# Performance work log

Measured on AMD Instinct MI355X. Metric: run time of the kernel, lower is better.

Reference implementation:

```python
import jax, jax.numpy as jnp
import numpy as np

# Sizes: N nodes, E directed edges, C input channels, H hidden channels.
N = 50000
E = 800000
C = 64
H = 64
EPS = 1e-5


def _bn(h, gamma, beta):
    # LazyBatchNorm: per-channel normalization over all rows (batch stats).
    m = h.mean(axis=0)
    v = ((h - m) ** 2).mean(axis=0)
    return (h - m) * jax.lax.rsqrt(v + EPS) * gamma + beta


def setup_inputs() -> dict:
    key = jax.random.key(0)
    ks = jax.random.split(key, 8)

    def glorot(k, shape):
        return jax.random.normal(k, shape, dtype=jnp.float32) / jnp.sqrt(jnp.float32(shape[0]))

    x = jax.random.normal(ks[0], (N, C), dtype=jnp.float32)
    edge_index = jax.random.randint(ks[1], (2, E), 0, N)
    return {
        "x": x,
        "edge_index": edge_index,
        "W_unite": glorot(ks[2], (2 * C, H)),
        "b_unite": jnp.zeros((H,), jnp.float32),
        "g1": jnp.ones((H,), jnp.float32),
        "be1": jnp.zeros((H,), jnp.float32),
        "W_gconv": glorot(ks[3], (2 * H, H)),
        "b_gconv": jnp.zeros((H,), jnp.float32),
        "g2": jnp.ones((H,), jnp.float32),
        "be2": jnp.zeros((H,), jnp.float32),
        "W_transfer": glorot(ks[4], (2 * H, H)),
        "b_transfer": jnp.zeros((H,), jnp.float32),
        "W_lin": glorot(ks[5], (H, H)),
        "b_lin": jnp.zeros((H,), jnp.float32),
        "g3": jnp.ones((H,), jnp.float32),
        "be3": jnp.zeros((H,), jnp.float32),
    }


def reference(x, edge_index, W_unite, b_unite, g1, be1, W_gconv, b_gconv, g2, be2,
              W_transfer, b_transfer, W_lin, b_lin, g3, be3):
    n = x.shape[0]
    src_e = edge_index[0]
    dst_e = edge_index[1]
    # linmaps1: ptensors0 -> ptensors1 with singleton reference domains (identity on data).
    # unite1: each node's domain becomes {node} U N(node). Row layout: first n rows
    # are self rows (atom i in domain i), then E rows (atom src in domain dst).
    self_idx = jnp.arange(n)
    rows_src = jnp.concatenate([self_idx, src_e])   # atom index per row
    rows_dom = jnp.concatenate([self_idx, dst_e])   # domain owner per row

    # --- unite1 (2 linmaps: gather + broadcast-of-domain-sum), then linear + BN + relu
    f = x[rows_src]                                           # [R, C] gather
    dsum = jax.ops.segment_sum(f, rows_dom, num_segments=n)   # [N, C]
    h = jnp.concatenate([f, dsum[rows_dom]], axis=-1) @ W_unite + b_unite  # [R, H]
    h = jax.nn.relu(_bn(h, g1, be1))
    # dropout1: identity in eval mode

    # --- higher graph conv: reduce each domain to order-0, aggregate over edges,
    # broadcast back and combine with local rows (2 maps), linear + BN + relu
    s = jax.ops.segment_sum(h, rows_dom, num_segments=n)          # [N, H] per-domain reduce
    msg = jax.ops.segment_sum(s[src_e], dst_e, num_segments=n)    # [N, H] neighborhood sum
    h2 = jnp.concatenate([h, msg[rows_dom]], axis=-1) @ W_gconv + b_gconv  # [R, H]
    h2 = jax.nn.relu(_bn(h2, g2, be2))
    # dropout2: identity

    # --- transfer back to ptensors0 (singleton domains): per-atom reduce over all rows
    # referencing that atom + the atom's own self row (2 maps), linear + BN + relu.
    # NOTE: the source reuses batchnorm2 here (it is assigned twice in __init__).
    agg = jax.ops.segment_sum(h2, rows_src, num_segments=n)       # [N, H]
    t = jnp.concatenate([h2[:n], agg], axis=-1) @ W_transfer + b_transfer  # [N, H]
    t = jax.nn.relu(_bn(t, g2, be2))
    # dropout3: identity

    # --- final linear + relu, BN + relu
    out = jax.nn.relu(t @ W_lin + b_lin)
    out = jax.nn.relu(_bn(out, g3, be3))
    # dropout4: identity
    return out
```

## Files before the change

kernel.cpp:

```cpp
#include <hip/hip_runtime.h>
#include <cstdint>
#include <math.h>

#define NN 50000
#define EE 800000
#define RR 850000
#define NT_N 3125
#define NT_R 53125
#define NBLK_H2 2048
#define NBLK_MM 512
#define CHUNK 512
#define NCH 98

typedef short  bf16x8 __attribute__((ext_vector_type(8)));
typedef float  f32x4  __attribute__((ext_vector_type(4)));

__device__ __forceinline__ float bf2f(unsigned short b) {
    unsigned int u = ((unsigned int)b) << 16;
    return __builtin_bit_cast(float, u);
}
__device__ __forceinline__ unsigned short f2bf(float f) {
    unsigned int u = __builtin_bit_cast(unsigned int, f);
    u = u + 0x7fffu + ((u >> 16) & 1u);
    return (unsigned short)(u >> 16);
}
__device__ __forceinline__ void atomAddD(double* p, double v) { unsafeAtomicAdd(p, v); }
__device__ __forceinline__ int atomAddI(int* p, int v) { return atomicAdd(p, v); }

__device__ __forceinline__ void split8(const float* p, bf16x8& hi, bf16x8& lo) {
    f32x4 v0 = *reinterpret_cast<const f32x4*>(p);
    f32x4 v1 = *reinterpret_cast<const f32x4*>(p + 4);
#pragma unroll
    for (int j = 0; j < 4; j++) {
        unsigned short h0 = f2bf(v0[j]);
        hi[j] = (short)h0; lo[j] = (short)f2bf(v0[j] - bf2f(h0));
        unsigned short h1 = f2bf(v1[j]);
        hi[4 + j] = (short)h1; lo[4 + j] = (short)f2bf(v1[j] - bf2f(h1));
    }
}
__device__ __forceinline__ void split8r(const float* v, bf16x8& hi, bf16x8& lo) {
#pragma unroll
    for (int j = 0; j < 8; j++) {
        unsigned short h = f2bf(v[j]);
        hi[j] = (short)h; lo[j] = (short)f2bf(v[j] - bf2f(h));
    }
}

template <bool RELU, bool STATS>
__device__ __forceinline__ void epi_tile(float* wl, int lane, const f32x4* acc,
                                         const float* bv, float* __restrict__ gout,
                                         int tile, double* ssum, double* ssq) {
    const int m = lane & 15, quad = lane >> 4;
#pragma unroll
    for (int ct = 0; ct < 4; ct++)
#pragma unroll
        for (int i = 0; i < 4; i++) {
            float val = acc[ct][i] + bv[ct];
            if (RELU) val = fmaxf(val, 0.f);
            wl[(quad * 4 + i) * 68 + ct * 16 + m] = val;
            if (STATS) { ssum[ct] += (double)val; ssq[ct] += (double)val * (double)val; }
        }
    asm volatile("s_waitcnt lgkmcnt(0)" ::: "memory");
#pragma unroll
    for (int j = 0; j < 4; j++) {
        int row = j * 4 + quad;
        f32x4 vv = *reinterpret_cast<const f32x4*>(wl + row * 68 + m * 4);
        *reinterpret_cast<f32x4*>(gout + ((size_t)(tile << 4) + row) * 64 + m * 4) = vv;
    }
}

__device__ __forceinline__ void epi_tile_b16(float* wl, int lane, const f32x4* acc,
                                             unsigned short* __restrict__ gout, int tile) {
    const int m = lane & 15, quad = lane >> 4;
#pragma unroll
    for (int ct = 0; ct < 4; ct++)
#pragma unroll
        for (int i = 0; i < 4; i++)
            wl[(quad * 4 + i) * 68 + ct * 16 + m] = acc[ct][i];
    asm volatile("s_waitcnt lgkmcnt(0)" ::: "memory");
#pragma unroll
    for (int j = 0; j < 4; j++) {
        int row = j * 4 + quad;
        f32x4 vv = *reinterpret_cast<const f32x4*>(wl + row * 68 + m * 4);
        unsigned int p0 = (unsigned int)f2bf(vv[0]) | ((unsigned int)f2bf(vv[1]) << 16);
        unsigned int p1 = (unsigned int)f2bf(vv[2]) | ((unsigned int)f2bf(vv[3]) << 16);
        uint2 pk; pk.x = p0; pk.y = p1;
        *reinterpret_cast<uint2*>(gout + ((size_t)(tile << 4) + row) * 64 + m * 4) = pk;
    }
}

__device__ __forceinline__ void stats_block_out(float* ldsbase, int lane, int wid,
                                                const double* ssum, const double* ssq,
                                                double* __restrict__ part) {
    const int m = lane & 15, quad = lane >> 4;
    double* dl = (double*)ldsbase;
    __syncthreads();
#pragma unroll
    for (int ct = 0; ct < 4; ct++) {
        double sv = ssum[ct], qv = ssq[ct];
        sv += __shfl_xor(sv, 16, 64); sv += __shfl_xor(sv, 32, 64);
        qv += __shfl_xor(qv, 16, 64); qv += __shfl_xor(qv, 32, 64);
        if (quad == 0) {
            dl[wid * 128 + ct * 16 + m]      = sv;
            dl[wid * 128 + 64 + ct * 16 + m] = qv;
        }
    }
    __syncthreads();
    int tid = wid * 64 + lane;
    if (tid < 128) {
        double tot = dl[tid] + dl[128 + tid] + dl[256 + tid] + dl[384 + tid];
        part[(size_t)blockIdx.x * 128 + tid] = tot;
    }
}

__global__ void k_red(const double* __restrict__ p, int nblk, double* __restrict__ raw) {
    int t = threadIdx.x;
    double acc = 0.0;
    for (int b = blockIdx.x; b < nblk; b += gridDim.x)
        acc += p[(size_t)b * 128 + t];
    atomAddD(&raw[t], acc);
}

__global__ void k_deg(const int* __restrict__ ei, int* __restrict__ od, int* __restrict__ id) {
    int e = blockIdx.x * 256 + threadIdx.x;
    atomAddI(&od[ei[e]], 1);
    atomAddI(&id[ei[EE + e]], 1);
}

__global__ void k_xc(const float* __restrict__ x, unsigned short* __restrict__ xb) {
    int i = blockIdx.x * 256 + threadIdx.x;
    xb[i] = f2bf(x[i]);
}

__global__ void k_scanA(const int* __restrict__ id, const int* __restrict__ od,
                        int* __restrict__ csum) {
    int arr = blockIdx.x / NCH;
    int ch  = blockIdx.x % NCH;
    const int* cnt = arr ? od : id;
    int t = threadIdx.x;
    int i0 = ch * CHUNK + t;
    int s = 0;
    if (i0 < NN) s += cnt[i0];
    if (i0 + 256 < NN && (t + 256) < CHUNK) s += cnt[i0 + 256];
#pragma unroll
    for (int d = 1; d < 64; d <<= 1) s += __shfl_xor(s, d, 64);
    __shared__ int ws[4];
    if ((t & 63) == 0) ws[t >> 6] = s;
    __syncthreads();
    if (t == 0) csum[arr * NCH + ch] = ws[0] + ws[1] + ws[2] + ws[3];
}

__global__ void k_scanB(int* __restrict__ csum) {
    __shared__ int part[256];
    int t = threadIdx.x;
    int arr = t >> 7, slot = t & 127;
    int v = (slot < NCH) ? csum[arr * NCH + slot] : 0;
    part[t] = v;
    __syncthreads();
#pragma unroll
    for (int d = 1; d < 128; d <<= 1) {
        int val = (slot >= d) ? part[t - d] : 0;
        __syncthreads();
        part[t] += val;
        __syncthreads();
    }
    if (slot < NCH)
        csum[arr * NCH + slot] = (slot == 0) ? 0 : part[t - 1];
}

__global__ void k_scanC(const int* __restrict__ id, const int* __restrict__ od,
                        const int* __restrict__ csum,
                        int* __restrict__ off, int* __restrict__ cursor,
                        int* __restrict__ off_s, int* __restrict__ cursor_s) {
    int arr = blockIdx.x / NCH;
    int ch  = blockIdx.x % NCH;
    const int* cnt = arr ? od : id;
    int* o  = arr ? off_s : off;
    int* cu = arr ? cursor_s : cursor;
    int t = threadIdx.x;
    int idx = ch * CHUNK + 2 * t;
    int e0 = 0, e1 = 0;
    if (idx < NN)     e0 = cnt[idx];
    if (idx + 1 < NN) e1 = cnt[idx + 1];
    int p = e0 + e1;
    int lane = t & 63;
    int incl = p;
#pragma unroll
    for (int d = 1; d < 64; d <<= 1) {
        int v = __shfl_up(incl, d, 64);
        if (lane >= d) incl += v;
    }
    __shared__ int wsum[4];
    if (lane == 63) wsum[t >> 6] = incl;
    __syncthreads();
    int w = t >> 6;
    int wbase = 0;
#pragma unroll
    for (int i = 0; i < 4; i++) if (i < w) wbase += wsum[i];
    int base = csum[arr * NCH + ch] + wbase + (incl - p);
    if (idx < NN)     { o[idx]     = base;      cu[idx]     = base; }
    if (idx + 1 < NN) { o[idx + 1] = base + e0; cu[idx + 1] = base + e0; }
    if (blockIdx.x == 0 && t == 0) { off[NN] = EE; off_s[NN] = EE; }
}

__global__ void k_fill(const int* __restrict__ ei, int* __restrict__ cursor,
                       unsigned int* __restrict__ sd_s) {
    int e = blockIdx.x * 256 + threadIdx.x;
    int s = ei[e], d = ei[EE + e];
    int p = atomAddI(&cursor[d], 1);
    sd_s[p] = (unsigned int)s | ((unsigned int)d << 16);
}

__global__ void k_fill2(const unsigned int* __restrict__ sd_s, int* __restrict__ cursor_s,
                        int* __restrict__ perm_s) {
    int p = blockIdx.x * 256 + threadIdx.x;
    int s = (int)(sd_s[p] & 0xFFFFu);
    int q = atomAddI(&cursor_s[s], 1);
    perm_s[q] = p;
}

__global__ void k_dsum_csr(const float* __restrict__ x, const unsigned short* __restrict__ xb,
                           const int* __restrict__ off,
                           const unsigned int* __restrict__ sd_s, float* __restrict__ dsum) {
    int team = (blockIdx.x * 256 + threadIdx.x) >> 6;
    int c = threadIdx.x & 63;
    float a[16];
#pragma unroll
    for (int j = 0; j < 16; j++) a[j] = 0.f;
    a[0] = x[(size_t)team * 64 + c];
    int e = off[team], e1 = off[team + 1];
    for (; e + 15 < e1; e += 16)
#pragma unroll
        for (int j = 0; j < 16; j++) a[j] += bf2f(xb[(size_t)(sd_s[e + j] & 0xFFFFu) * 64 + c]);
    for (; e + 3 < e1; e += 4)
#pragma unroll
        for (int j = 0; j < 4; j++) a[j] += bf2f(xb[(size_t)(sd_s[e + j] & 0xFFFFu) * 64 + c]);
    for (; e < e1; e++) a[0] += bf2f(xb[(size_t)(sd_s[e] & 0xFFFFu) * 64 + c]);
#pragma unroll
    for (int j = 0; j < 8; j++) a[j] += a[j + 8];
#pragma unroll
    for (int j = 0; j < 4; j++) a[j] += a[j + 4];
    dsum[(size_t)team * 64 + c] = (a[0] + a[1]) + (a[2] + a[3]);
}

__global__ void k_uv3(const float* __restrict__ x, const float* __restrict__ dsum,
                      const float* __restrict__ W, unsigned short* __restrict__ ub,
                      float* __restrict__ v, float* __restrict__ u2) {
    __shared__ float lds[4][16 * 68];
    const int lane = threadIdx.x & 63;
    const int wid = threadIdx.x >> 6;
    const int m = lane & 15, quad = lane >> 4;
    const int gwave = (blockIdx.x * blockDim.x + threadIdx.x) >> 6;
    const int nwaves = (gridDim.x * blockDim.x) >> 6;
    float* wl = lds[wid];

    bf16x8 wfh[4][4], wfl[4][4];
#pragma unroll
    for (int kk = 0; kk < 4; kk++)
#pragma unroll
        for (int ct = 0; ct < 4; ct++) {
            float wv[8];
#pragma unroll
            for (int j = 0; j < 8; j++)
                wv[j] = W[(kk * 32 + quad * 8 + j) * 64 + ct * 16 + m];
            split8r(wv, wfh[kk][ct], wfl[kk][ct]);
        }
    float zb[4] = {0.f, 0.f, 0.f, 0.f};

    for (int tile = gwave; tile < NT_N; tile += nwaves) {
        const int r = (tile << 4) + m;
        bf16x8 ah[4], al[4];
        split8(x    + (size_t)r * 64 + quad * 8,      ah[0], al[0]);
        split8(x    + (size_t)r * 64 + 32 + quad * 8, ah[1], al[1]);
        split8(dsum + (size_t)r * 64 + quad * 8,      ah[2], al[2]);
        split8(dsum + (size_t)r * 64 + 32 + quad * 8, ah[3], al[3]);

        f32x4 zero = {0.f, 0.f, 0.f, 0.f};
        f32x4 aU[4], aV[4], aU2[4];
#pragma unroll
        for (int ct = 0; ct < 4; ct++) {
            aU[ct] = zero; aV[ct] = zero; aU2[ct] = zero;
#pragma unroll
            for (int kk = 0; kk < 2; kk++) {
                aU[ct]  = __builtin_amdgcn_mfma_f32_16x16x32_bf16(al[kk],   wfh[kk][ct],   aU[ct],  0, 0, 0);
                aU[ct]  = __builtin_amdgcn_mfma_f32_16x16x32_bf16(ah[kk],   wfl[kk][ct],   aU[ct],  0, 0, 0);
                aU[ct]  = __builtin_amdgcn_mfma_f32_16x16x32_bf16(ah[kk],   wfh[kk][ct],   aU[ct],  0, 0, 0);
                aV[ct]  = __builtin_amdgcn_mfma_f32_16x16x32_bf16(al[kk+2], wfh[kk+2][ct], aV[ct],  0, 0, 0);
                aV[ct]  = __builtin_amdgcn_mfma_f32_16x16x32_bf16(ah[kk+2], wfl[kk+2][ct], aV[ct],  0, 0, 0);
                aV[ct]  = __builtin_amdgcn_mfma_f32_16x16x32_bf16(ah[kk+2], wfh[kk+2][ct], aV[ct],  0, 0, 0);
                aU2[ct] = __builtin_amdgcn_mfma_f32_16x16x32_bf16(al[kk+2], wfh[kk][ct],   aU2[ct], 0, 0, 0);
                aU2[ct] = __builtin_amdgcn_mfma_f32_16x16x32_bf16(ah[kk+2], wfl[kk][ct],   aU2[ct], 0, 0, 0);
                aU2[ct] = __builtin_amdgcn_mfma_f32_16x16x32_bf16(ah[kk+2], wfh[kk][ct],   aU2[ct], 0, 0, 0);
            }
        }
        epi_tile_b16(wl, lane, aU, ub, tile);
        epi_tile<false, false>(wl, lane, aV,  zb, v,  tile, nullptr, nullptr);
        epi_tile<false, false>(wl, lane, aU2, zb, u2, tile, nullptr, nullptr);
    }
}

__global__ void k_stats1a(const unsigned short* __restrict__ ub, const float* __restrict__ v,
                          const float* __restrict__ u2, const int* __restrict__ od,
                          const int* __restrict__ id, double* __restrict__ stats_raw) {
    __shared__ double lsum[4][64], lsq[4][64];
    int tid = threadIdx.x, c = tid & 63, w = tid >> 6;
    double a1 = 0.0, a2 = 0.0;
    for (int n = blockIdx.x * 4 + w; n < NN; n += gridDim.x * 4) {
        double uu = (double)bf2f(ub[(size_t)n * 64 + c]);
        double vv = v[(size_t)n * 64 + c];
        double uu2 = u2[(size_t)n * 64 + c];
        double wod = 1.0 + od[n], wid = 1.0 + id[n];
        a1 += wod * uu + wid * vv;
        a2 += wod * uu * uu + wid * vv * vv + 2.0 * vv * uu2;
    }
    lsum[w][c] = a1; lsq[w][c] = a2;
    __syncthreads();
    if (w == 0) {
        a1 = lsum[0][c] + lsum[1][c] + lsum[2][c] + lsum[3][c];
        a2 = lsq[0][c] + lsq[1][c] + lsq[2][c] + lsq[3][c];
        atomAddD(&stats_raw[c], a1);
        atomAddD(&stats_raw[64 + c], a2);
    }
}

__global__ void k_fin1(const double* __restrict__ raw, const float* __restrict__ b,
                       float* __restrict__ fin, double inv_cnt) {
    int c = threadIdx.x;
    double m1 = raw[c] * inv_cnt;
    double var = raw[64 + c] * inv_cnt - m1 * m1;
    if (var < 0.0) var = 0.0;
    fin[c] = (float)(m1 + (double)b[c]);
    fin[64 + c] = (float)(1.0 / sqrt(var + 1e-5));
}

__global__ void k_fin(const double* __restrict__ raw, float* __restrict__ fin, double inv_cnt) {
    int c = threadIdx.x;
    double mean = raw[c] * inv_cnt;
    double var = raw[64 + c] * inv_cnt - mean * mean;
    if (var < 0.0) var = 0.0;
    fin[c] = (float)mean;
    fin[64 + c] = (float)(1.0 / sqrt(var + 1e-5));
}

__global__ void k_s1h(const unsigned short* __restrict__ ub, const float* __restrict__ v,
                      const int* __restrict__ off, const unsigned int* __restrict__ sd_s,
                      const float* __restrict__ b_un, const float* __restrict__ fin,
                      const float* __restrict__ g1, const float* __restrict__ be1,
                      unsigned short* __restrict__ stb, unsigned short* __restrict__ hb) {
    int team = (blockIdx.x * 256 + threadIdx.x) >> 6;
    int c = threadIdx.x & 63;
    float sc = fin[64 + c] * g1[c];
    float tsh = (b_un[c] - fin[c]) * sc + be1[c];
    float vn = v[(size_t)team * 64 + c];
    float a[16];
#pragma unroll
    for (int j = 0; j < 16; j++) a[j] = 0.f;
    float hs = fmaxf((bf2f(ub[(size_t)team * 64 + c]) + vn) * sc + tsh, 0.f);
    a[0] = hs;
    hb[(size_t)team * 64 + c] = f2bf(hs);
    int e = off[team], e1 = off[team + 1];
    for (; e + 15 < e1; e += 16)
#pragma unroll
        for (int j = 0; j < 16; j++) {
            float h = fmaxf((bf2f(ub[(size_t)(sd_s[e + j] & 0xFFFFu) * 64 + c]) + vn) * sc + tsh, 0.f);
            a[j] += h;
            hb[(size_t)(NN + e + j) * 64 + c] = f2bf(h);
        }
    for (; e + 3 < e1; e += 4)
#pragma unroll
        for (int j = 0; j < 4; j++) {
            float h = fmaxf((bf2f(ub[(size_t)(sd_s[e + j] & 0xFFFFu) * 64 + c]) + vn) * sc + tsh, 0.f);
            a[j] += h;
            hb[(size_t)(NN + e + j) * 64 + c] = f2bf(h);
        }
    for (; e < e1; e++) {
        float h = fmaxf((bf2f(ub[(size_t)(sd_s[e] & 0xFFFFu) * 64 + c]) + vn) * sc + tsh, 0.f);
        a[0] += h;
        hb[(size_t)(NN + e) * 64 + c] = f2bf(h);
    }
#pragma unroll
    for (int j = 0; j < 8; j++) a[j] += a[j + 8];
#pragma unroll
    for (int j = 0; j < 4; j++) a[j] += a[j + 4];
    stb[(size_t)team * 64 + c] = f2bf((a[0] + a[1]) + (a[2] + a[3]));
}

__global__ void k_msg_csr(const int* __restrict__ off, const unsigned int* __restrict__ sd_s,
                          const unsigned short* __restrict__ stb, float* __restrict__ msg) {
    int team = (blockIdx.x * 256 + threadIdx.x) >> 6;
    int c = threadIdx.x & 63;
    float a[16];
#pragma unroll
    for (int j = 0; j < 16; j++) a[j] = 0.f;
    int e = off[team], e1 = off[team + 1];
    for (; e + 15 < e1; e += 16)
#pragma unroll
        for (int j = 0; j < 16; j++) a[j] += bf2f(stb[(size_t)(sd_s[e + j] & 0xFFFFu) * 64 + c]);
    for (; e + 3 < e1; e += 4)
#pragma unroll
        for (int j = 0; j < 4; j++) a[j] += bf2f(stb[(size_t)(sd_s[e + j] & 0xFFFFu) * 64 + c]);
    for (; e < e1; e++) a[0] += bf2f(stb[(size_t)(sd_s[e] & 0xFFFFu) * 64 + c]);
#pragma unroll
    for (int j = 0; j < 8; j++) a[j] += a[j + 8];
#pragma unroll
    for (int j = 0; j < 4; j++) a[j] += a[j + 4];
    msg[(size_t)team * 64 + c] = (a[0] + a[1]) + (a[2] + a[3]);
}

__global__ void k_mb(const float* __restrict__ in, float* __restrict__ outp,
                     const float* __restrict__ W) {
    __shared__ float lds[4][16 * 68];
    const int lane = threadIdx.x & 63;
    const int wid = threadIdx.x >> 6;
    const int m = lane & 15, quad = lane >> 4;
    const int gwave = (blockIdx.x * blockDim.x + threadIdx.x) >> 6;
    const int nwaves = (gridDim.x * blockDim.x) >> 6;
    float* wl = lds[wid];

    bf16x8 wfh[2][4], wfl[2][4];
#pragma unroll
    for (int kk = 0; kk < 2; kk++)
#pragma unroll
        for (int ct = 0; ct < 4; ct++) {
            float wv[8];
#pragma unroll
            for (int j = 0; j < 8; j++)
                wv[j] = W[(kk * 32 + quad * 8 + j) * 64 + ct * 16 + m];
            split8r(wv, wfh[kk][ct], wfl[kk][ct]);
        }
    float zb[4] = {0.f, 0.f, 0.f, 0.f};

    for (int tile = gwave; tile < NT_N; tile += nwaves) {
        const int r = (tile << 4) + m;
        bf16x8 ah[2], al[2];
        split8(in + (size_t)r * 64 + quad * 8,      ah[0], al[0]);
        split8(in + (size_t)r * 64 + 32 + quad * 8, ah[1], al[1]);

        f32x4 zero = {0.f, 0.f, 0.f, 0.f};
        f32x4 acc[4];
#pragma unroll
        for (int ct = 0; ct < 4; ct++) {
            acc[ct] = zero;
#pragma unroll
            for (int kk = 0; kk < 2; kk++) {
                acc[ct] = __builtin_amdgcn_mfma_f32_16x16x32_bf16(al[kk], wfh[kk][ct], acc[ct], 0, 0, 0);
                acc[ct] = __builtin_amdgcn_mfma_f32_16x16x32_bf16(ah[kk], wfl[kk][ct], acc[ct], 0, 0, 0);
                acc[ct] = __builtin_amdgcn_mfma_f32_16x16x32_bf16(ah[kk], wfh[kk][ct], acc[ct], 0, 0, 0);
            }
        }
        epi_tile<false, false>(wl, lane, acc, zb, outp, tile, nullptr, nullptr);
    }
}

__global__ void k_h2(const unsigned short* __restrict__ hb, unsigned short* __restrict__ h2b,
                     const float* __restrict__ mb, const unsigned int* __restrict__ sd_s,
                     const float* __restrict__ W, const float* __restrict__ b_gc,
                     double* __restrict__ part) {
    __shared__ float lds[4][16 * 68];
    const int lane = threadIdx.x & 63;
    const int wid = threadIdx.x >> 6;
    const int m = lane & 15, quad = lane >> 4;
    const int gwave = (blockIdx.x * blockDim.x + threadIdx.x) >> 6;
    const int nwaves = (gridDim.x * blockDim.x) >> 6;
    float* wl = lds[wid];

    bf16x8 wfh[2][4], wfl[2][4];
#pragma unroll
    for (int kk = 0; kk < 2; kk++)
#pragma unroll
        for (int ct = 0; ct < 4; ct++) {
            float wv[8];
#pragma unroll
            for (int j = 0; j < 8; j++)
                wv[j] = W[(kk * 32 + quad * 8 + j) * 64 + ct * 16 + m];
            split8r(wv, wfh[kk][ct], wfl[kk][ct]);
        }

    float bv[4];
#pragma unroll
    for (int ct = 0; ct < 4; ct++) bv[ct] = b_gc[ct * 16 + m];

    double ssum[4] = {0,0,0,0}, ssq[4] = {0,0,0,0};

    for (int tile = gwave; tile < NT_R; tile += nwaves) {
        const int r = (tile << 4) + m;
        int dm = (tile < NT_N) ? r : (int)(sd_s[r - NN] >> 16);

        bf16x8 ah[2];
        ah[0] = *reinterpret_cast<const bf16x8*>(hb + (size_t)r * 64 + quad * 8);
        ah[1] = *reinterpret_cast<const bf16x8*>(hb + (size_t)r * 64 + 32 + quad * 8);

        f32x4 zero = {0.f, 0.f, 0.f, 0.f};
        f32x4 acc[4];
#pragma unroll
        for (int ct = 0; ct < 4; ct++) {
            acc[ct] = zero;
#pragma unroll
            for (int kk = 0; kk < 2; kk++) {
                acc[ct] = __builtin_amdgcn_mfma_f32_16x16x32_bf16(ah[kk], wfl[kk][ct], acc[ct], 0, 0, 0);
                acc[ct] = __builtin_amdgcn_mfma_f32_16x16x32_bf16(ah[kk], wfh[kk][ct], acc[ct], 0, 0, 0);
            }
        }

#pragma unroll
        for (int i = 0; i < 4; i++) {
            int dmv = __shfl(dm, (lane & 48) + quad * 4 + i, 64);
#pragma unroll
            for (int ct = 0; ct < 4; ct++) {
                float val = acc[ct][i] + bv[ct] + mb[(size_t)dmv * 64 + ct * 16 + m];
                wl[(quad * 4 + i) * 68 + ct * 16 + m] = val;
                ssum[ct] += (double)val;
                ssq[ct]  += (double)val * (double)val;
            }
        }
        asm volatile("s_waitcnt lgkmcnt(0)" ::: "memory");
#pragma unroll
        for (int j = 0; j < 4; j++) {
            int row = j * 4 + quad;
            f32x4 vv = *reinterpret_cast<const f32x4*>(wl + row * 68 + m * 4);
            unsigned int p0 = (unsigned int)f2bf(vv[0]) | ((unsigned int)f2bf(vv[1]) << 16);
            unsigned int p1 = (unsigned int)f2bf(vv[2]) | ((unsigned int)f2bf(vv[3]) << 16);
            uint2 pk; pk.x = p0; pk.y = p1;
            *reinterpret_cast<uint2*>(h2b + ((size_t)(tile << 4) + row) * 64 + m * 4) = pk;
        }
    }

    stats_block_out(&lds[0][0], lane, wid, ssum, ssq, part);
}

__global__ void k_agg_csr(const unsigned short* __restrict__ h2b, const int* __restrict__ off_s,
                          const int* __restrict__ perm_s, const float* __restrict__ fin2,
                          const float* __restrict__ g2, const float* __restrict__ be2,
                          float* __restrict__ agg) {
    int n = (blockIdx.x * 256 + threadIdx.x) >> 6;
    int c = threadIdx.x & 63;
    float sc = fin2[64 + c] * g2[c];
    float sh = be2[c] - fin2[c] * sc;
    float a[16];
#pragma unroll
    for (int j = 0; j < 16; j++) a[j] = 0.f;
    a[0] = fmaxf(bf2f(h2b[(size_t)n * 64 + c]) * sc + sh, 0.f);
    int q = off_s[n], q1 = off_s[n + 1];
    for (; q + 15 < q1; q += 16)
#pragma unroll
        for (int j = 0; j < 16; j++) {
            float hv = bf2f(h2b[(size_t)(NN + perm_s[q + j]) * 64 + c]);
            a[j] += fmaxf(hv * sc + sh, 0.f);
        }
    for (; q + 3 < q1; q += 4)
#pragma unroll
        for (int j = 0; j < 4; j++) {
            float hv = bf2f(h2b[(size_t)(NN + perm_s[q + j]) * 64 + c]);
            a[j] += fmaxf(hv * sc + sh, 0.f);
        }
    for (; q < q1; q++) {
        float hv = bf2f(h2b[(size_t)(NN + perm_s[q]) * 64 + c]);
        a[0] += fmaxf(hv * sc + sh, 0.f);
    }
#pragma unroll
    for (int j = 0; j < 8; j++) a[j] += a[j + 8];
#pragma unroll
    for (int j = 0; j < 4; j++) a[j] += a[j + 4];
    agg[(size_t)n * 64 + c] = (a[0] + a[1]) + (a[2] + a[3]);
}

__global__ void k_mm3(const unsigned short* __restrict__ h2b, const float* __restrict__ agg,
                      const float* __restrict__ W, const float* __restrict__ bias,
                      const float* __restrict__ fin2, const float* __restrict__ g2,
                      const float* __restrict__ be2,
                      float* __restrict__ outp, double* __restrict__ part) {
    __shared__ float lds[4][16 * 68];
    const int lane = threadIdx.x & 63;
    const int wid = threadIdx.x >> 6;
    const int m = lane & 15, quad = lane >> 4;
    const int gwave = (blockIdx.x * blockDim.x + threadIdx.x) >> 6;
    const int nwaves = (gridDim.x * blockDim.x) >> 6;
    float* wl = lds[wid];

    bf16x8 wfh[4][4], wfl[4][4];
#pragma unroll
    for (int kk = 0; kk < 4; kk++)
#pragma unroll
        for (int ct = 0; ct < 4; ct++) {
            float wv[8];
#pragma unroll
            for (int j = 0; j < 8; j++)
                wv[j] = W[(kk * 32 + quad * 8 + j) * 64 + ct * 16 + m];
            split8r(wv, wfh[kk][ct], wfl[kk][ct]);
        }

    float bv[4];
#pragma unroll
    for (int ct = 0; ct < 4; ct++) bv[ct] = bias[ct * 16 + m];

    float s2f[2][8], t2f[2][8];
#pragma unroll
    for (int kk = 0; kk < 2; kk++)
#pragma unroll
        for (int j = 0; j < 8; j++) {
            int c = kk * 32 + quad * 8 + j;
            float sc = fin2[64 + c] * g2[c];
            s2f[kk][j] = sc;
            t2f[kk][j] = be2[c] - fin2[c] * sc;
        }

    double ssum[4] = {0,0,0,0}, ssq[4] = {0,0,0,0};

    for (int tile = gwave; tile < NT_N; tile += nwaves) {
        const int r = (tile << 4) + m;
        bf16x8 ah[4], al[4];
#pragma unroll
        for (int kk = 0; kk < 2; kk++) {
            bf16x8 hv = *reinterpret_cast<const bf16x8*>(h2b + (size_t)r * 64 + kk * 32 + quad * 8);
            float tv[8];
#pragma unroll
            for (int j = 0; j < 8; j++) {
                float f = bf2f((unsigned short)hv[j]);
                tv[j] = fmaxf(f * s2f[kk][j] + t2f[kk][j], 0.f);
            }
            split8r(tv, ah[kk], al[kk]);
        }
        split8(agg + (size_t)r * 64 + quad * 8,      ah[2], al[2]);
        split8(agg + (size_t)r * 64 + 32 + quad * 8, ah[3], al[3]);

        f32x4 zero = {0.f, 0.f, 0.f, 0.f};
        f32x4 acc[4];
#pragma unroll
        for (int ct = 0; ct < 4; ct++) {
            acc[ct] = zero;
#pragma unroll
            for (int kk = 0; kk < 4; kk++)
                acc[ct] = __builtin_amdgcn_mfma_f32_16x16x32_bf16(al[kk], wfh[kk][ct], acc[ct], 0, 0, 0);
#pragma unroll
            for (int kk = 0; kk < 4; kk++)
                acc[ct] = __builtin_amdgcn_mfma_f32_16x16x32_bf16(ah[kk], wfl[kk][ct], acc[ct], 0, 0, 0);
#pragma unroll
            for (int kk = 0; kk < 4; kk++)
                acc[ct] = __builtin_amdgcn_mfma_f32_16x16x32_bf16(ah[kk], wfh[kk][ct], acc[ct], 0, 0, 0);
        }

        epi_tile<false, true>(wl, lane, acc, bv, outp, tile, ssum, ssq);
    }

    stats_block_out(&lds[0][0], lane, wid, ssum, ssq, part);
}

__global__ void k_mm4(const float* __restrict__ tpre, const float* __restrict__ W,
                      const float* __restrict__ bias, const float* __restrict__ fin3,
                      const float* __restrict__ g2, const float* __restrict__ be2,
                      float* __restrict__ outp, double* __restrict__ part) {
    __shared__ float lds[4][16 * 68];
    const int lane = threadIdx.x & 63;
    const int wid = threadIdx.x >> 6;
    const int m = lane & 15, quad = lane >> 4;
    const int gwave = (blockIdx.x * blockDim.x + threadIdx.x) >> 6;
    const int nwaves = (gridDim.x * blockDim.x) >> 6;
    float* wl = lds[wid];

    bf16x8 wfh[2][4], wfl[2][4];
#pragma unroll
    for (int kk = 0; kk < 2; kk++)
#pragma unroll
        for (int ct = 0; ct < 4; ct++) {
            float wv[8];
#pragma unroll
            for (int j = 0; j < 8; j++)
                wv[j] = W[(kk * 32 + quad * 8 + j) * 64 + ct * 16 + m];
            split8r(wv, wfh[kk][ct], wfl[kk][ct]);
        }

    float bv[4];
#pragma unroll
    for (int ct = 0; ct < 4; ct++) bv[ct] = bias[ct * 16 + m];

    float sc[2][8], sh[2][8];
#pragma unroll
    for (int kk = 0; kk < 2; kk++)
#pragma unroll
        for (int j = 0; j < 8; j++) {
            int c = kk * 32 + quad * 8 + j;
            float s = fin3[64 + c] * g2[c];
            sc[kk][j] = s;
            sh[kk][j] = be2[c] - fin3[c] * s;
        }

    double ssum[4] = {0,0,0,0}, ssq[4] = {0,0,0,0};

    for (int tile = gwave; tile < NT_N; tile += nwaves) {
        const int r = (tile << 4) + m;
        bf16x8 ah[2], al[2];
#pragma unroll
        for (int kk = 0; kk < 2; kk++) {
            f32x4 v0 = *reinterpret_cast<const f32x4*>(tpre + (size_t)r * 64 + kk * 32 + quad * 8);
            f32x4 v1 = *reinterpret_cast<const f32x4*>(tpre + (size_t)r * 64 + kk * 32 + quad * 8 + 4);
            float tv[8];
#pragma unroll
            for (int j = 0; j < 4; j++) {
                tv[j]     = fmaxf(v0[j] * sc[kk][j]     + sh[kk][j],     0.f);
                tv[4 + j] = fmaxf(v1[j] * sc[kk][4 + j] + sh[kk][4 + j], 0.f);
            }
            split8r(tv, ah[kk], al[kk]);
        }

        f32x4 zero = {0.f, 0.f, 0.f, 0.f};
        f32x4 acc[4];
#pragma unroll
        for (int ct = 0; ct < 4; ct++) {
            acc[ct] = zero;
#pragma unroll
            for (int kk = 0; kk < 2; kk++) {
                acc[ct] = __builtin_amdgcn_mfma_f32_16x16x32_bf16(al[kk], wfh[kk][ct], acc[ct], 0, 0, 0);
                acc[ct] = __builtin_amdgcn_mfma_f32_16x16x32_bf16(ah[kk], wfl[kk][ct], acc[ct], 0, 0, 0);
                acc[ct] = __builtin_amdgcn_mfma_f32_16x16x32_bf16(ah[kk], wfh[kk][ct], acc[ct], 0, 0, 0);
            }
        }

        epi_tile<true, true>(wl, lane, acc, bv, outp, tile, ssum, ssq);
    }

    stats_block_out(&lds[0][0], lane, wid, ssum, ssq, part);
}

__global__ void k_out(const float* __restrict__ op, const float* __restrict__ fin,
                      const float* __restrict__ g, const float* __restrict__ be,
                      float* __restrict__ out) {
    int i = blockIdx.x * 256 + threadIdx.x;
    int c = i & 63;
    out[i] = fmaxf((op[i] - fin[c]) * fin[64 + c] * g[c] + be[c], 0.f);
}

extern "C" void kernel_launch(void* const* d_in, const int* in_sizes, int n_in,
                              void* d_out, int out_size, void* d_ws, size_t ws_size,
                              hipStream_t stream) {
    const float* x    = (const float*)d_in[0];
    const int*   ei   = (const int*)d_in[1];
    const float* W_un = (const float*)d_in[2];
    const float* b_un = (const float*)d_in[3];
    const float* g1   = (const float*)d_in[4];
    const float* be1  = (const float*)d_in[5];
    const float* W_gc = (const float*)d_in[6];
    const float* b_gc = (const float*)d_in[7];
    const float* g2   = (const float*)d_in[8];
    const float* be2  = (const float*)d_in[9];
    const float* W_tr = (const float*)d_in[10];
    const float* b_tr = (const float*)d_in[11];
    const float* W_li = (const float*)d_in[12];
    const float* b_li = (const float*)d_in[13];
    const float* g3   = (const float*)d_in[14];
    const float* be3  = (const float*)d_in[15];

    float* ws = (float*)d_ws;
    const size_t FN = (size_t)NN * 64;
    const size_t FR = (size_t)RR * 64;
    float* P0 = ws;
    float* P1 = ws + FN;
    float* P2 = ws + 2 * FN;
    float* H  = ws + 3 * FN;
    unsigned short* ub   = (unsigned short*)P0;
    float* v      = P1;
    unsigned short* stb  = (unsigned short*)P2;
    int*   csum   = (int*)P2;
    float* dsum   = H;
    float* u2     = H + FN;
    unsigned short* xb16 = (unsigned short*)(H + 2 * FN);
    unsigned short* hb  = (unsigned short*)H;
    unsigned short* h2b = (unsigned short*)H + FR;
    float* msg    = P0;
    float* agg    = P1;
    float* tpre   = P2;
    float* outpre = P0;
    double* part_h2 = (double*)P2;
    double* part_m3 = (double*)P0;
    double* part_m4 = (double*)P1;
    double*       stats_raw = (double*)(H + FR);
    int*          od        = (int*)(stats_raw + 512);
    int*          id        = od + NN;
    int*          off       = id + NN;
    int*          cursor    = off + NN + 1;
    int*          off_s     = cursor + NN;
    int*          cursor_s  = off_s + NN + 1;
    unsigned int* sd_s      = (unsigned int*)(cursor_s + NN);
    int*          perm_s    = (int*)(sd_s + EE);
    float*        stats_fin = (float*)(perm_s + EE);

    hipMemsetAsync(stats_raw, 0, 512 * sizeof(double) + 2 * NN * sizeof(int), stream);

    k_deg  <<<3125, 256, 0, stream>>>(ei, od, id);
    k_xc   <<<12500, 256, 0, stream>>>(x, xb16);
    k_scanA<<<2 * NCH, 256, 0, stream>>>(id, od, csum);
    k_scanB<<<1, 256, 0, stream>>>(csum);
    k_scanC<<<2 * NCH, 256, 0, stream>>>(id, od, csum, off, cursor, off_s, cursor_s);
    k_fill <<<3125, 256, 0, stream>>>(ei, cursor, sd_s);
    k_fill2<<<3125, 256, 0, stream>>>(sd_s, cursor_s, perm_s);

    k_dsum_csr<<<12500, 256, 0, stream>>>(x, xb16, off, sd_s, dsum);
    k_uv3<<<512, 256, 0, stream>>>(x, dsum, W_un, ub, v, u2);

    k_stats1a<<<256, 256, 0, stream>>>(ub, v, u2, od, id, stats_raw + 0);
    k_fin1<<<1, 64, 0, stream>>>(stats_raw + 0, b_un, stats_fin + 0, 1.0 / (double)RR);
    k_s1h<<<12500, 256, 0, stream>>>(ub, v, off, sd_s, b_un, stats_fin + 0, g1, be1,
                                     stb, hb);
    k_msg_csr<<<12500, 256, 0, stream>>>(off, sd_s, stb, msg);
    k_mb<<<512, 256, 0, stream>>>(msg, msg, W_gc + 64 * 64);

    k_h2<<<NBLK_H2, 256, 0, stream>>>(hb, h2b, msg, sd_s, W_gc, b_gc, part_h2);
    k_red<<<32, 128, 0, stream>>>(part_h2, NBLK_H2, stats_raw + 128);
    k_fin<<<1, 64, 0, stream>>>(stats_raw + 128, stats_fin + 128, 1.0 / (double)RR);
    k_agg_csr<<<12500, 256, 0, stream>>>(h2b, off_s, perm_s, stats_fin + 128, g2, be2, agg);

    k_mm3<<<NBLK_MM, 256, 0, stream>>>(h2b, agg, W_tr, b_tr, stats_fin + 128, g2, be2,
                                       tpre, part_m3);
    k_red<<<16, 128, 0, stream>>>(part_m3, NBLK_MM, stats_raw + 256);
    k_fin<<<1, 64, 0, stream>>>(stats_raw + 256, stats_fin + 256, 1.0 / (double)NN);

    k_mm4<<<NBLK_MM, 256, 0, stream>>>(tpre, W_li, b_li, stats_fin + 256, g2, be2,
                                       outpre, part_m4);
    k_red<<<16, 128, 0, stream>>>(part_m4, NBLK_MM, stats_raw + 384);
    k_fin<<<1, 64, 0, stream>>>(stats_raw + 384, stats_fin + 384, 1.0 / (double)NN);

    k_out<<<12500, 256, 0, stream>>>(outpre, stats_fin + 384, g3, be3, (float*)d_out);
}
```

Before: 716.7 us.

## Fuse degree count with bf16 convert, fold BN1 stats into uv3, store agg as bf16

```diff
diff --git a/kernel.cpp b/kernel.cpp
--- a/kernel.cpp
+++ b/kernel.cpp
@@ -121,15 +121,14 @@
     atomAddD(&raw[t], acc);
 }
 
-__global__ void k_deg(const int* __restrict__ ei, int* __restrict__ od, int* __restrict__ id) {
-    int e = blockIdx.x * 256 + threadIdx.x;
-    atomAddI(&od[ei[e]], 1);
-    atomAddI(&id[ei[EE + e]], 1);
-}
-
-__global__ void k_xc(const float* __restrict__ x, unsigned short* __restrict__ xb) {
+__global__ void k_degx(const int* __restrict__ ei, int* __restrict__ od, int* __restrict__ id,
+                       const float* __restrict__ x, unsigned short* __restrict__ xb) {
     int i = blockIdx.x * 256 + threadIdx.x;
     xb[i] = f2bf(x[i]);
+    if (i < EE) {
+        atomAddI(&od[ei[i]], 1);
+        atomAddI(&id[ei[EE + i]], 1);
+    }
 }
 
 __global__ void k_scanA(const int* __restrict__ id, const int* __restrict__ od,
@@ -244,15 +243,17 @@
 }
 
 __global__ void k_uv3(const float* __restrict__ x, const float* __restrict__ dsum,
-                      const float* __restrict__ W, unsigned short* __restrict__ ub,
-                      float* __restrict__ v, float* __restrict__ u2) {
+                      const float* __restrict__ W,
+                      const int* __restrict__ od, const int* __restrict__ id,
+                      unsigned short* __restrict__ ub, float* __restrict__ v,
+                      double* __restrict__ part) {
     __shared__ float lds[4][16 * 68];
     const int lane = threadIdx.x & 63;
-    const int wid = threadIdx.x >> 6;
+    const int wid_ = threadIdx.x >> 6;
     const int m = lane & 15, quad = lane >> 4;
     const int gwave = (blockIdx.x * blockDim.x + threadIdx.x) >> 6;
     const int nwaves = (gridDim.x * blockDim.x) >> 6;
-    float* wl = lds[wid];
+    float* wl = lds[wid_];
 
     bf16x8 wfh[4][4], wfl[4][4];
 #pragma unroll
@@ -266,6 +267,7 @@
             split8r(wv, wfh[kk][ct], wfl[kk][ct]);
         }
     float zb[4] = {0.f, 0.f, 0.f, 0.f};
+    double ssum[4] = {0,0,0,0}, ssq[4] = {0,0,0,0};
 
     for (int tile = gwave; tile < NT_N; tile += nwaves) {
         const int r = (tile << 4) + m;
@@ -293,34 +295,24 @@
                 aU2[ct] = __builtin_amdgcn_mfma_f32_16x16x32_bf16(ah[kk+2], wfh[kk][ct],   aU2[ct], 0, 0, 0);
             }
         }
+
+#pragma unroll
+        for (int i = 0; i < 4; i++) {
+            int r2 = (tile << 4) + quad * 4 + i;
+            double wod = 1.0 + od[r2], wgt = 1.0 + id[r2];
+#pragma unroll
+            for (int ct = 0; ct < 4; ct++) {
+                double uu = aU[ct][i], vv = aV[ct][i], u2v = aU2[ct][i];
+                ssum[ct] += wod * uu + wgt * vv;
+                ssq[ct]  += wod * uu * uu + wgt * vv * vv + 2.0 * vv * u2v;
+            }
+        }
+
         epi_tile_b16(wl, lane, aU, ub, tile);
-        epi_tile<false, false>(wl, lane, aV,  zb, v,  tile, nullptr, nullptr);
-        epi_tile<false, false>(wl, lane, aU2, zb, u2, tile, nullptr, nullptr);
-    }
-}
-
-__global__ void k_stats1a(const unsigned short* __restrict__ ub, const float* __restrict__ v,
-                          const float* __restrict__ u2, const int* __restrict__ od,
-                          const int* __restrict__ id, double* __restrict__ stats_raw) {
-    __shared__ double lsum[4][64], lsq[4][64];
-    int tid = threadIdx.x, c = tid & 63, w = tid >> 6;
-    double a1 = 0.0, a2 = 0.0;
-    for (int n = blockIdx.x * 4 + w; n < NN; n += gridDim.x * 4) {
-        double uu = (double)bf2f(ub[(size_t)n * 64 + c]);
-        double vv = v[(size_t)n * 64 + c];
-        double uu2 = u2[(size_t)n * 64 + c];
-        double wod = 1.0 + od[n], wid = 1.0 + id[n];
-        a1 += wod * uu + wid * vv;
-        a2 += wod * uu * uu + wid * vv * vv + 2.0 * vv * uu2;
-    }
-    lsum[w][c] = a1; lsq[w][c] = a2;
-    __syncthreads();
-    if (w == 0) {
-        a1 = lsum[0][c] + lsum[1][c] + lsum[2][c] + lsum[3][c];
-        a2 = lsq[0][c] + lsq[1][c] + lsq[2][c] + lsq[3][c];
-        atomAddD(&stats_raw[c], a1);
-        atomAddD(&stats_raw[64 + c], a2);
-    }
+        epi_tile<false, false>(wl, lane, aV, zb, v, tile, nullptr, nullptr);
+    }
+
+    stats_block_out(&lds[0][0], lane, wid_, ssum, ssq, part);
 }
 
 __global__ void k_fin1(const double* __restrict__ raw, const float* __restrict__ b,
@@ -531,7 +523,7 @@
 __global__ void k_agg_csr(const unsigned short* __restrict__ h2b, const int* __restrict__ off_s,
                           const int* __restrict__ perm_s, const float* __restrict__ fin2,
                           const float* __restrict__ g2, const float* __restrict__ be2,
-                          float* __restrict__ agg) {
+                          unsigned short* __restrict__ aggb) {
     int n = (blockIdx.x * 256 + threadIdx.x) >> 6;
     int c = threadIdx.x & 63;
     float sc = fin2[64 + c] * g2[c];
@@ -561,10 +553,10 @@
     for (int j = 0; j < 8; j++) a[j] += a[j + 8];
 #pragma unroll
     for (int j = 0; j < 4; j++) a[j] += a[j + 4];
-    agg[(size_t)n * 64 + c] = (a[0] + a[1]) + (a[2] + a[3]);
-}
-
-__global__ void k_mm3(const unsigned short* __restrict__ h2b, const float* __restrict__ agg,
+    aggb[(size_t)n * 64 + c] = f2bf((a[0] + a[1]) + (a[2] + a[3]));
+}
+
+__global__ void k_mm3(const unsigned short* __restrict__ h2b, const unsigned short* __restrict__ aggb,
                       const float* __restrict__ W, const float* __restrict__ bias,
                       const float* __restrict__ fin2, const float* __restrict__ g2,
                       const float* __restrict__ be2,
@@ -608,7 +600,7 @@
 
     for (int tile = gwave; tile < NT_N; tile += nwaves) {
         const int r = (tile << 4) + m;
-        bf16x8 ah[4], al[4];
+        bf16x8 ah[4], al[2];
 #pragma unroll
         for (int kk = 0; kk < 2; kk++) {
             bf16x8 hv = *reinterpret_cast<const bf16x8*>(h2b + (size_t)r * 64 + kk * 32 + quad * 8);
@@ -620,8 +612,8 @@
             }
             split8r(tv, ah[kk], al[kk]);
         }
-        split8(agg + (size_t)r * 64 + quad * 8,      ah[2], al[2]);
-        split8(agg + (size_t)r * 64 + 32 + quad * 8, ah[3], al[3]);
+        ah[2] = *reinterpret_cast<const bf16x8*>(aggb + (size_t)r * 64 + quad * 8);
+        ah[3] = *reinterpret_cast<const bf16x8*>(aggb + (size_t)r * 64 + 32 + quad * 8);
 
         f32x4 zero = {0.f, 0.f, 0.f, 0.f};
         f32x4 acc[4];
@@ -629,7 +621,7 @@
         for (int ct = 0; ct < 4; ct++) {
             acc[ct] = zero;
 #pragma unroll
-            for (int kk = 0; kk < 4; kk++)
+            for (int kk = 0; kk < 2; kk++)
                 acc[ct] = __builtin_amdgcn_mfma_f32_16x16x32_bf16(al[kk], wfh[kk][ct], acc[ct], 0, 0, 0);
 #pragma unroll
             for (int kk = 0; kk < 4; kk++)
@@ -760,13 +752,13 @@
     float* v      = P1;
     unsigned short* stb  = (unsigned short*)P2;
     int*   csum   = (int*)P2;
+    double* part_uv = (double*)P2;
     float* dsum   = H;
-    float* u2     = H + FN;
-    unsigned short* xb16 = (unsigned short*)(H + 2 * FN);
+    unsigned short* xb16 = (unsigned short*)(H + FN);
     unsigned short* hb  = (unsigned short*)H;
     unsigned short* h2b = (unsigned short*)H + FR;
     float* msg    = P0;
-    float* agg    = P1;
+    unsigned short* aggb = (unsigned short*)P1;
     float* tpre   = P2;
     float* outpre = P0;
     double* part_h2 = (double*)P2;
@@ -785,8 +777,7 @@
 
     hipMemsetAsync(stats_raw, 0, 512 * sizeof(double) + 2 * NN * sizeof(int), stream);
 
-    k_deg  <<<3125, 256, 0, stream>>>(ei, od, id);
-    k_xc   <<<12500, 256, 0, stream>>>(x, xb16);
+    k_degx <<<12500, 256, 0, stream>>>(ei, od, id, x, xb16);
     k_scanA<<<2 * NCH, 256, 0, stream>>>(id, od, csum);
     k_scanB<<<1, 256, 0, stream>>>(csum);
     k_scanC<<<2 * NCH, 256, 0, stream>>>(id, od, csum, off, cursor, off_s, cursor_s);
@@ -794,10 +785,10 @@
     k_fill2<<<3125, 256, 0, stream>>>(sd_s, cursor_s, perm_s);
 
     k_dsum_csr<<<12500, 256, 0, stream>>>(x, xb16, off, sd_s, dsum);
-    k_uv3<<<512, 256, 0, stream>>>(x, dsum, W_un, ub, v, u2);
-
-    k_stats1a<<<256, 256, 0, stream>>>(ub, v, u2, od, id, stats_raw + 0);
+    k_uv3<<<NBLK_MM, 256, 0, stream>>>(x, dsum, W_un, od, id, ub, v, part_uv);
+    k_red<<<16, 128, 0, stream>>>(part_uv, NBLK_MM, stats_raw + 0);
     k_fin1<<<1, 64, 0, stream>>>(stats_raw + 0, b_un, stats_fin + 0, 1.0 / (double)RR);
+
     k_s1h<<<12500, 256, 0, stream>>>(ub, v, off, sd_s, b_un, stats_fin + 0, g1, be1,
                                      stb, hb);
     k_msg_csr<<<12500, 256, 0, stream>>>(off, sd_s, stb, msg);
@@ -806,9 +797,9 @@
     k_h2<<<NBLK_H2, 256, 0, stream>>>(hb, h2b, msg, sd_s, W_gc, b_gc, part_h2);
     k_red<<<32, 128, 0, stream>>>(part_h2, NBLK_H2, stats_raw + 128);
     k_fin<<<1, 64, 0, stream>>>(stats_raw + 128, stats_fin + 128, 1.0 / (double)RR);
-    k_agg_csr<<<12500, 256, 0, stream>>>(h2b, off_s, perm_s, stats_fin + 128, g2, be2, agg);
-
-    k_mm3<<<NBLK_MM, 256, 0, stream>>>(h2b, agg, W_tr, b_tr, stats_fin + 128, g2, be2,
+    k_agg_csr<<<12500, 256, 0, stream>>>(h2b, off_s, perm_s, stats_fin + 128, g2, be2, aggb);
+
+    k_mm3<<<NBLK_MM, 256, 0, stream>>>(h2b, aggb, W_tr, b_tr, stats_fin + 128, g2, be2,
                                        tpre, part_m3);
     k_red<<<16, 128, 0, stream>>>(part_m3, NBLK_MM, stats_raw + 256);
     k_fin<<<1, 64, 0, stream>>>(stats_raw + 256, stats_fin + 256, 1.0 / (double)NN);
```

After: 689.0 us. 3.9% less time.
